# Kernel tuning notes

Hardware: AMD Instinct MI355X
Metric: run time of the kernel (lower is better)

The kernel has to match this reference:

```python
import jax, jax.numpy as jnp
import numpy as np

B, N, D = 8, 1024, 768
H, HD = 12, 64


def setup_inputs() -> dict:
    key = jax.random.key(0)
    ks = jax.random.split(key, 9)
    return {
        "x": jax.random.normal(ks[0], (B, N, D), dtype=jnp.float32),
        "Wq": jax.random.normal(ks[1], (H, HD, HD), dtype=jnp.float32) * (HD ** -0.5),
        "Wk": jax.random.normal(ks[2], (H, HD, HD), dtype=jnp.float32) * (HD ** -0.5),
        "Wv": jax.random.normal(ks[3], (H, HD, HD), dtype=jnp.float32) * (HD ** -0.5),
        "bq": jax.random.normal(ks[4], (H, HD), dtype=jnp.float32) * 0.02,
        "bk": jax.random.normal(ks[5], (H, HD), dtype=jnp.float32) * 0.02,
        "bv": jax.random.normal(ks[6], (H, HD), dtype=jnp.float32) * 0.02,
        "Wo": jax.random.normal(ks[7], (D, D), dtype=jnp.float32) * (D ** -0.5),
        "bo": jnp.zeros((D,), dtype=jnp.float32),
    }


def reference(x, Wq, Wk, Wv, bq, bk, bv, Wo, bo):
    # x: [B, N, D]; split into H heads of size HD along the feature dim
    b, n, d = x.shape
    h, hd = Wq.shape[0], Wq.shape[1]
    xh = x.reshape(b, n, h, hd)
    # per-head linear projections (stacked nn.Linear(head_dim, head_dim))
    q = jnp.einsum('bnhd,hde->bhne', xh, Wq) + bq[None, :, None, :]
    k = jnp.einsum('bnhd,hde->bhne', xh, Wk) + bk[None, :, None, :]
    v = jnp.einsum('bnhd,hde->bhne', xh, Wv) + bv[None, :, None, :]
    # NOTE: faithful quirk - scale uses FULL dim, not head_dim
    scale = d ** -0.5
    scores = jnp.einsum('bhid,bhjd->bhij', q, k) * scale  # [B,H,N,N]
    attn = jax.nn.softmax(scores, axis=-1)
    out = jnp.einsum('bhij,bhjd->bhid', attn, v)  # [B,H,N,HD]
    out = out.transpose(0, 2, 1, 3).reshape(b, n, d)  # concat heads
    return out @ Wo.T + bo  # wO: nn.Linear(dim, dim)
```

## Files before the change

### kernel.cpp

```cpp
#include <hip/hip_runtime.h>


typedef __attribute__((ext_vector_type(8))) short short8;
typedef __attribute__((ext_vector_type(4))) float floatx4;

#define MFMA16(a, b, c) __builtin_amdgcn_mfma_f32_16x16x32_bf16((a), (b), (c), 0, 0, 0)

#if __has_builtin(__builtin_amdgcn_exp2f)
#define EXP2(x) __builtin_amdgcn_exp2f(x)
#else
#define EXP2(x) __expf(0.6931471805599453f * (x))
#endif
#if __has_builtin(__builtin_amdgcn_rcpf)
#define RCP(x) __builtin_amdgcn_rcpf(x)
#else
#define RCP(x) (1.0f / (x))
#endif

__device__ __forceinline__ unsigned short f2bf(float f) {
    union { float f; unsigned int i; } c;
    c.f = f;
    unsigned int i = c.i;
    return (unsigned short)((i + 0x7fffu + ((i >> 16) & 1u)) >> 16);
}
__device__ __forceinline__ unsigned short f2bf_trunc(float f) {
    union { float f; unsigned int i; } c;
    c.f = f;
    return (unsigned short)(c.i >> 16);
}

__global__ __launch_bounds__(256) void prep_weights(
    const float* __restrict__ Wq, const float* __restrict__ Wk,
    const float* __restrict__ Wv, const float* __restrict__ Wo,
    unsigned short* __restrict__ Wqt, unsigned short* __restrict__ Wkt,
    unsigned short* __restrict__ Wvt, unsigned short* __restrict__ Wob)
{
    int tid = blockIdx.x * 256 + threadIdx.x;
    if (tid < 49152) {
        int h = tid >> 12, r = tid & 4095;
        int e = r >> 6, k = r & 63;
        int src = h * 4096 + k * 64 + e, dst = h * 4096 + e * 64 + k;
        Wqt[dst] = f2bf(Wq[src]);
        Wkt[dst] = f2bf(Wk[src]);
        Wvt[dst] = f2bf(Wv[src]);
    }
    for (int i = tid; i < 589824; i += 147456) Wob[i] = f2bf(Wo[i]);
}

__global__ __launch_bounds__(256) void qkv_proj(
    const float* __restrict__ x,
    const unsigned short* __restrict__ Wqt, const unsigned short* __restrict__ Wkt,
    const unsigned short* __restrict__ Wvt,
    const float* __restrict__ bq, const float* __restrict__ bk,
    const float* __restrict__ bv,
    unsigned short* __restrict__ Q, unsigned short* __restrict__ K,
    unsigned short* __restrict__ Vt)
{
    __shared__ __align__(16) unsigned short xlds[64 * 72];
    __shared__ __align__(16) unsigned short vlds[64 * 72];

    const int bh = blockIdx.y;
    const int b = bh / 12, h = bh % 12;
    const int wave = threadIdx.x >> 6, lane = threadIdx.x & 63;
    const int lrow = lane & 15, quad = lane >> 4;
    const int row0 = blockIdx.x * 64;
    const float scale = 0.052058776672f;

    {
        const int tr = threadIdx.x >> 4;
        const int tc = (threadIdx.x & 15) * 4;
        #pragma unroll
        for (int rr = 0; rr < 4; ++rr) {
            const int r = tr + rr * 16;
            const float* src = x + ((size_t)(b * 1024 + row0 + r)) * 768
                               + h * 64 + tc;
            float4 f = *(const float4*)src;
            unsigned short pkd[4];
            pkd[0] = f2bf(f.x); pkd[1] = f2bf(f.y);
            pkd[2] = f2bf(f.z); pkd[3] = f2bf(f.w);
            *(uint2*)&xlds[r * 72 + tc] = *(uint2*)pkd;
        }
    }
    __syncthreads();

    short8 xb0 = *(const short8*)&xlds[(wave * 16 + lrow) * 72 + quad * 8];
    short8 xb1 = *(const short8*)&xlds[(wave * 16 + lrow) * 72 + 32 + quad * 8];

    const floatx4 zero = { 0.f, 0.f, 0.f, 0.f };

    const unsigned short* Wm[2] = { Wqt + h * 4096, Wkt + h * 4096 };
    const float* bm[2] = { bq + h * 64, bk + h * 64 };
    unsigned short* Om[2] = {
        Q + ((size_t)bh * 1024 + row0 + wave * 16 + lrow) * 64,
        K + ((size_t)bh * 1024 + row0 + wave * 16 + lrow) * 64 };
    #pragma unroll
    for (int m = 0; m < 2; ++m) {
        const unsigned short* W = Wm[m];
        #pragma unroll
        for (int t = 0; t < 4; ++t) {
            short8 wa0 = *(const short8*)(W + (t * 16 + lrow) * 64 + quad * 8);
            short8 wa1 = *(const short8*)(W + (t * 16 + lrow) * 64 + 32 + quad * 8);
            floatx4 acc = zero;
            acc = MFMA16(wa0, xb0, acc);
            acc = MFMA16(wa1, xb1, acc);
            float4 bias = *(const float4*)(bm[m] + t * 16 + quad * 4);
            const float bs[4] = { bias.x, bias.y, bias.z, bias.w };
            unsigned short pkd[4];
            #pragma unroll
            for (int r = 0; r < 4; ++r) {
                float v = acc[r] + bs[r];
                if (m == 0) v *= scale;
                pkd[r] = f2bf(v);
            }
            *(uint2*)(Om[m] + t * 16 + quad * 4) = *(uint2*)pkd;
        }
    }

    {
        const unsigned short* W = Wvt + h * 4096;
        const float* bvh = bv + h * 64;
        #pragma unroll
        for (int t = 0; t < 4; ++t) {
            short8 wa0 = *(const short8*)(W + (t * 16 + lrow) * 64 + quad * 8);
            short8 wa1 = *(const short8*)(W + (t * 16 + lrow) * 64 + 32 + quad * 8);
            floatx4 acc = zero;
            acc = MFMA16(wa0, xb0, acc);
            acc = MFMA16(wa1, xb1, acc);
            float4 bias = *(const float4*)(bvh + t * 16 + quad * 4);
            const float bs[4] = { bias.x, bias.y, bias.z, bias.w };
            #pragma unroll
            for (int r = 0; r < 4; ++r)
                vlds[(t * 16 + quad * 4 + r) * 72 + wave * 16 + lrow]
                    = f2bf(acc[r] + bs[r]);
        }
    }
    __syncthreads();
    {
        const int er = threadIdx.x >> 2;
        const int sc = threadIdx.x & 3;
        short8 v0 = *(const short8*)&vlds[er * 72 + sc * 16];
        short8 v1 = *(const short8*)&vlds[er * 72 + sc * 16 + 8];
        unsigned short* dst = Vt + (size_t)bh * 65536 + (size_t)er * 1024
                              + row0 + sc * 16;
        *(short8*)dst = v0;
        *(short8*)(dst + 8) = v1;
    }
}

__global__ __launch_bounds__(256) void attn_kernel(
    const unsigned short* __restrict__ Q, const unsigned short* __restrict__ K,
    const unsigned short* __restrict__ Vt, unsigned short* __restrict__ AO)
{
    __shared__ __align__(16) unsigned short Klds[64 * 72];
    __shared__ __align__(16) unsigned short Vlds[64 * 72];

    const int bh = (int)blockIdx.x + ((int)blockIdx.y >> 3) * 8;
    const int qb = blockIdx.y & 7;
    const int b = bh / 12, h = bh % 12;
    const int wave = threadIdx.x >> 6, lane = threadIdx.x & 63;
    const int lrow = lane & 15, quad = lane >> 4;
    const int qrow0 = qb * 128 + wave * 32;

    const unsigned short* Qb = Q + (size_t)bh * 65536;
    const unsigned short* Kb = K + (size_t)bh * 65536;
    const unsigned short* Vb = Vt + (size_t)bh * 65536;

    const int tch = threadIdx.x & 7, trow = threadIdx.x >> 3;
    const int slot0 = ((trow & 4) << 2) | ((trow >> 3) << 2) | (trow & 3);

    short8 aq[2][2];
    #pragma unroll
    for (int mm = 0; mm < 2; ++mm) {
        const unsigned short* qr = Qb + (size_t)(qrow0 + mm * 16 + lrow) * 64;
        aq[mm][0] = *(const short8*)(qr + quad * 8);
        aq[mm][1] = *(const short8*)(qr + 32 + quad * 8);
    }

    const floatx4 zero = { 0.f, 0.f, 0.f, 0.f };
    float part[2] = { 0.f, 0.f };
    floatx4 Oacc[2][4];
    #pragma unroll
    for (int mm = 0; mm < 2; ++mm)
        #pragma unroll
        for (int t = 0; t < 4; ++t) Oacc[mm][t] = zero;

    short8 kpre[2], vpre[2];
    kpre[0] = *(const short8*)(Kb + (size_t)trow * 64 + tch * 8);
    kpre[1] = *(const short8*)(Kb + (size_t)(trow + 32) * 64 + tch * 8);
    vpre[0] = *(const short8*)(Vb + (size_t)trow * 1024 + tch * 8);
    vpre[1] = *(const short8*)(Vb + (size_t)(trow + 32) * 1024 + tch * 8);

    for (int jt = 0; jt < 16; ++jt) {
        *(short8*)&Klds[slot0 * 72 + tch * 8] = kpre[0];
        *(short8*)&Klds[(slot0 + 32) * 72 + tch * 8] = kpre[1];
        *(short8*)&Vlds[trow * 72 + tch * 8] = vpre[0];
        *(short8*)&Vlds[(trow + 32) * 72 + tch * 8] = vpre[1];
        __syncthreads();

        {
            const int jn = ((jt + 1) & 15) * 64;
            kpre[0] = *(const short8*)(Kb + (size_t)(jn + trow) * 64 + tch * 8);
            kpre[1] = *(const short8*)(Kb + (size_t)(jn + trow + 32) * 64 + tch * 8);
            vpre[0] = *(const short8*)(Vb + (size_t)trow * 1024 + jn + tch * 8);
            vpre[1] = *(const short8*)(Vb + (size_t)(trow + 32) * 1024 + jn + tch * 8);
        }

        #pragma unroll
        for (int w = 0; w < 2; ++w) {
            short8 kA[2][2];
            #pragma unroll
            for (int tau = 0; tau < 2; ++tau) {
                int kr = w * 32 + tau * 16 + lrow;
                kA[tau][0] = *(const short8*)&Klds[kr * 72 + quad * 8];
                kA[tau][1] = *(const short8*)&Klds[kr * 72 + 32 + quad * 8];
            }
            short8 vA[4];
            #pragma unroll
            for (int t = 0; t < 4; ++t)
                vA[t] = *(const short8*)&Vlds[(t * 16 + lrow) * 72
                                              + w * 32 + quad * 8];

            #pragma unroll
            for (int mm = 0; mm < 2; ++mm) {
                floatx4 s0 = zero, s1 = zero;
                s0 = MFMA16(kA[0][0], aq[mm][0], s0);
                s0 = MFMA16(kA[0][1], aq[mm][1], s0);
                s1 = MFMA16(kA[1][0], aq[mm][0], s1);
                s1 = MFMA16(kA[1][1], aq[mm][1], s1);

                short8 pk;
                #pragma unroll
                for (int r = 0; r < 4; ++r) {
                    float p0 = EXP2(s0[r]);
                    float p1 = EXP2(s1[r]);
                    part[mm] += p0 + p1;
                    pk[r] = (short)f2bf_trunc(p0);
                    pk[4 + r] = (short)f2bf_trunc(p1);
                }
                #pragma unroll
                for (int t = 0; t < 4; ++t)
                    Oacc[mm][t] = MFMA16(vA[t], pk, Oacc[mm][t]);
            }
        }
        __syncthreads();
    }

    #pragma unroll
    for (int mm = 0; mm < 2; ++mm) {
        float ts = part[mm];
        ts += __shfl_xor(ts, 16);
        ts += __shfl_xor(ts, 32);
        float inv = RCP(ts);
        unsigned short* orow = AO
            + ((size_t)(b * 1024 + qrow0 + mm * 16 + lrow)) * 768 + h * 64;
        #pragma unroll
        for (int t = 0; t < 4; ++t) {
            unsigned short pkd[4];
            #pragma unroll
            for (int r = 0; r < 4; ++r)
                pkd[r] = f2bf(Oacc[mm][t][r] * inv);
            *(uint2*)(orow + t * 16 + quad * 4) = *(uint2*)pkd;
        }
    }
}

__global__ __launch_bounds__(256) void out_proj(
    const unsigned short* __restrict__ AO, const unsigned short* __restrict__ Wob,
    const float* __restrict__ bo, float* __restrict__ Y)
{
    __shared__ __align__(16) unsigned short Alds[128 * 72];
    __shared__ __align__(16) unsigned short Blds[64 * 72];

    const int wave = threadIdx.x >> 6, lane = threadIdx.x & 63;
    const int lrow = lane & 15, quad = lane >> 4;
    const int row0 = blockIdx.x * 128;
    const int c0 = blockIdx.y * 64;
    const int wrow = (wave >> 1) * 64, wcol = (wave & 1) * 32;

    const int tch = threadIdx.x & 7, trow = threadIdx.x >> 3;

    const floatx4 zero = { 0.f, 0.f, 0.f, 0.f };
    floatx4 acc[2][4];
    #pragma unroll
    for (int u = 0; u < 2; ++u)
        #pragma unroll
        for (int t = 0; t < 4; ++t) acc[u][t] = zero;

    short8 apre[4], bpre[2];
    #pragma unroll
    for (int rr = 0; rr < 4; ++rr)
        apre[rr] = *(const short8*)(AO + (size_t)(row0 + trow + rr * 32) * 768
                                    + tch * 8);
    #pragma unroll
    for (int rr = 0; rr < 2; ++rr)
        bpre[rr] = *(const short8*)(Wob + (size_t)(c0 + trow + rr * 32) * 768
                                    + tch * 8);

    for (int k0 = 0; k0 < 768; k0 += 64) {
        #pragma unroll
        for (int rr = 0; rr < 4; ++rr)
            *(short8*)&Alds[(trow + rr * 32) * 72 + tch * 8] = apre[rr];
        #pragma unroll
        for (int rr = 0; rr < 2; ++rr)
            *(short8*)&Blds[(trow + rr * 32) * 72 + tch * 8] = bpre[rr];
        __syncthreads();

        {
            const int kn = (k0 + 64 < 768) ? k0 + 64 : 0;
            #pragma unroll
            for (int rr = 0; rr < 4; ++rr)
                apre[rr] = *(const short8*)(AO
                    + (size_t)(row0 + trow + rr * 32) * 768 + kn + tch * 8);
            #pragma unroll
            for (int rr = 0; rr < 2; ++rr)
                bpre[rr] = *(const short8*)(Wob
                    + (size_t)(c0 + trow + rr * 32) * 768 + kn + tch * 8);
        }

        #pragma unroll
        for (int kc = 0; kc < 2; ++kc) {
            short8 aoF[4], wF[2];
            #pragma unroll
            for (int t = 0; t < 4; ++t)
                aoF[t] = *(const short8*)&Alds[(wrow + t * 16 + lrow) * 72
                                               + kc * 32 + quad * 8];
            #pragma unroll
            for (int u = 0; u < 2; ++u)
                wF[u] = *(const short8*)&Blds[(wcol + u * 16 + lrow) * 72
                                              + kc * 32 + quad * 8];
            #pragma unroll
            for (int u = 0; u < 2; ++u)
                #pragma unroll
                for (int t = 0; t < 4; ++t)
                    acc[u][t] = MFMA16(wF[u], aoF[t], acc[u][t]);
        }
        __syncthreads();
    }

    #pragma unroll
    for (int u = 0; u < 2; ++u) {
        const int cb = c0 + wcol + u * 16 + quad * 4;
        float4 bias = *(const float4*)(bo + cb);
        const float bs[4] = { bias.x, bias.y, bias.z, bias.w };
        #pragma unroll
        for (int t = 0; t < 4; ++t) {
            const int row = row0 + wrow + t * 16 + lrow;
            float out[4];
            #pragma unroll
            for (int r = 0; r < 4; ++r) out[r] = acc[u][t][r] + bs[r];
            *(float4*)(Y + (size_t)row * 768 + cb) = *(float4*)out;
        }
    }
}

extern "C" void kernel_launch(void* const* d_in, const int* in_sizes, int n_in,
                              void* d_out, int out_size, void* d_ws, size_t ws_size,
                              hipStream_t stream)
{
    const float* x  = (const float*)d_in[0];
    const float* Wq = (const float*)d_in[1];
    const float* Wk = (const float*)d_in[2];
    const float* Wv = (const float*)d_in[3];
    const float* bq = (const float*)d_in[4];
    const float* bk = (const float*)d_in[5];
    const float* bv = (const float*)d_in[6];
    const float* Wo = (const float*)d_in[7];
    const float* bo = (const float*)d_in[8];

    unsigned short* Q   = (unsigned short*)d_ws;
    unsigned short* K   = Q + 6291456;
    unsigned short* Vt  = K + 6291456;
    unsigned short* AO  = Vt + 6291456;
    unsigned short* Wqt = AO + 6291456;
    unsigned short* Wkt = Wqt + 49152;
    unsigned short* Wvt = Wkt + 49152;
    unsigned short* Wob = Wvt + 49152;
    float* Y = (float*)d_out;

    prep_weights<<<dim3(576), 256, 0, stream>>>(Wq, Wk, Wv, Wo, Wqt, Wkt, Wvt, Wob);
    qkv_proj<<<dim3(16, 96), 256, 0, stream>>>(x, Wqt, Wkt, Wvt, bq, bk, bv, Q, K, Vt);
    attn_kernel<<<dim3(8, 96), 256, 0, stream>>>(Q, K, Vt, AO);
    out_proj<<<dim3(64, 12), 256, 0, stream>>>(AO, Wob, bo, Y);
}
```

Before: 169.9 us.

## Compute softmax row sums via MFMA with ones, packed bf16 cvt, wider out_proj tiles

In the attention kernel, the probability row sums are now accumulated with an extra MFMA against a bf16 ones vector instead of per-lane scalar adds plus cross-lane shuffles. The sum is taken over the bf16-rounded probabilities, which makes it consistent with what feeds the PV product. Probability conversion now uses the hardware packed v_cvt_pk_bf16_f32 instruction (round-to-nearest) instead of manual truncation. Separately, the output projection tile widens from 64 to 96 columns per block, cutting the grid from 12 to 8 column blocks, which gives more reuse per A load at the cost of more registers and LDS.

```diff
diff --git a/kernel.cpp b/kernel.cpp
--- a/kernel.cpp
+++ b/kernel.cpp
@@ -23,11 +23,6 @@
     unsigned int i = c.i;
     return (unsigned short)((i + 0x7fffu + ((i >> 16) & 1u)) >> 16);
 }
-__device__ __forceinline__ unsigned short f2bf_trunc(float f) {
-    union { float f; unsigned int i; } c;
-    c.f = f;
-    return (unsigned short)(c.i >> 16);
-}
 
 __global__ __launch_bounds__(256) void prep_weights(
     const float* __restrict__ Wq, const float* __restrict__ Wk,
@@ -177,7 +172,10 @@
     }
 
     const floatx4 zero = { 0.f, 0.f, 0.f, 0.f };
-    float part[2] = { 0.f, 0.f };
+    const short one_bf = (short)0x3F80;
+    const short8 ones8 = { one_bf, one_bf, one_bf, one_bf,
+                           one_bf, one_bf, one_bf, one_bf };
+    floatx4 Sacc[2] = { zero, zero };
     floatx4 Oacc[2][4];
     #pragma unroll
     for (int mm = 0; mm < 2; ++mm)
@@ -228,15 +226,20 @@
                 s1 = MFMA16(kA[1][0], aq[mm][0], s1);
                 s1 = MFMA16(kA[1][1], aq[mm][1], s1);
 
+                float p00 = EXP2(s0[0]), p01 = EXP2(s0[1]);
+                float p02 = EXP2(s0[2]), p03 = EXP2(s0[3]);
+                float p10 = EXP2(s1[0]), p11 = EXP2(s1[1]);
+                float p12 = EXP2(s1[2]), p13 = EXP2(s1[3]);
+                unsigned int w0, w1, w2, w3;
+                asm("v_cvt_pk_bf16_f32 %0, %1, %2" : "=v"(w0) : "v"(p00), "v"(p01));
+                asm("v_cvt_pk_bf16_f32 %0, %1, %2" : "=v"(w1) : "v"(p02), "v"(p03));
+                asm("v_cvt_pk_bf16_f32 %0, %1, %2" : "=v"(w2) : "v"(p10), "v"(p11));
+                asm("v_cvt_pk_bf16_f32 %0, %1, %2" : "=v"(w3) : "v"(p12), "v"(p13));
                 short8 pk;
-                #pragma unroll
-                for (int r = 0; r < 4; ++r) {
-                    float p0 = EXP2(s0[r]);
-                    float p1 = EXP2(s1[r]);
-                    part[mm] += p0 + p1;
-                    pk[r] = (short)f2bf_trunc(p0);
-                    pk[4 + r] = (short)f2bf_trunc(p1);
-                }
+                unsigned int* pw = (unsigned int*)&pk;
+                pw[0] = w0; pw[1] = w1; pw[2] = w2; pw[3] = w3;
+
+                Sacc[mm] = MFMA16(ones8, pk, Sacc[mm]);
                 #pragma unroll
                 for (int t = 0; t < 4; ++t)
                     Oacc[mm][t] = MFMA16(vA[t], pk, Oacc[mm][t]);
@@ -247,10 +250,7 @@
 
     #pragma unroll
     for (int mm = 0; mm < 2; ++mm) {
-        float ts = part[mm];
-        ts += __shfl_xor(ts, 16);
-        ts += __shfl_xor(ts, 32);
-        float inv = RCP(ts);
+        float inv = RCP(Sacc[mm][0]);
         unsigned short* orow = AO
             + ((size_t)(b * 1024 + qrow0 + mm * 16 + lrow)) * 768 + h * 64;
         #pragma unroll
@@ -269,30 +269,30 @@
     const float* __restrict__ bo, float* __restrict__ Y)
 {
     __shared__ __align__(16) unsigned short Alds[128 * 72];
-    __shared__ __align__(16) unsigned short Blds[64 * 72];
+    __shared__ __align__(16) unsigned short Blds[96 * 72];
 
     const int wave = threadIdx.x >> 6, lane = threadIdx.x & 63;
     const int lrow = lane & 15, quad = lane >> 4;
     const int row0 = blockIdx.x * 128;
-    const int c0 = blockIdx.y * 64;
-    const int wrow = (wave >> 1) * 64, wcol = (wave & 1) * 32;
+    const int c0 = blockIdx.y * 96;
+    const int wrow = (wave >> 1) * 64, wcol = (wave & 1) * 48;
 
     const int tch = threadIdx.x & 7, trow = threadIdx.x >> 3;
 
     const floatx4 zero = { 0.f, 0.f, 0.f, 0.f };
-    floatx4 acc[2][4];
-    #pragma unroll
-    for (int u = 0; u < 2; ++u)
+    floatx4 acc[3][4];
+    #pragma unroll
+    for (int u = 0; u < 3; ++u)
         #pragma unroll
         for (int t = 0; t < 4; ++t) acc[u][t] = zero;
 
-    short8 apre[4], bpre[2];
+    short8 apre[4], bpre[3];
     #pragma unroll
     for (int rr = 0; rr < 4; ++rr)
         apre[rr] = *(const short8*)(AO + (size_t)(row0 + trow + rr * 32) * 768
                                     + tch * 8);
     #pragma unroll
-    for (int rr = 0; rr < 2; ++rr)
+    for (int rr = 0; rr < 3; ++rr)
         bpre[rr] = *(const short8*)(Wob + (size_t)(c0 + trow + rr * 32) * 768
                                     + tch * 8);
 
@@ -301,7 +301,7 @@
         for (int rr = 0; rr < 4; ++rr)
             *(short8*)&Alds[(trow + rr * 32) * 72 + tch * 8] = apre[rr];
         #pragma unroll
-        for (int rr = 0; rr < 2; ++rr)
+        for (int rr = 0; rr < 3; ++rr)
             *(short8*)&Blds[(trow + rr * 32) * 72 + tch * 8] = bpre[rr];
         __syncthreads();
 
@@ -312,24 +312,24 @@
                 apre[rr] = *(const short8*)(AO
                     + (size_t)(row0 + trow + rr * 32) * 768 + kn + tch * 8);
             #pragma unroll
-            for (int rr = 0; rr < 2; ++rr)
+            for (int rr = 0; rr < 3; ++rr)
                 bpre[rr] = *(const short8*)(Wob
                     + (size_t)(c0 + trow + rr * 32) * 768 + kn + tch * 8);
         }
 
         #pragma unroll
         for (int kc = 0; kc < 2; ++kc) {
-            short8 aoF[4], wF[2];
+            short8 aoF[4], wF[3];
             #pragma unroll
             for (int t = 0; t < 4; ++t)
                 aoF[t] = *(const short8*)&Alds[(wrow + t * 16 + lrow) * 72
                                                + kc * 32 + quad * 8];
             #pragma unroll
-            for (int u = 0; u < 2; ++u)
+            for (int u = 0; u < 3; ++u)
                 wF[u] = *(const short8*)&Blds[(wcol + u * 16 + lrow) * 72
                                               + kc * 32 + quad * 8];
             #pragma unroll
-            for (int u = 0; u < 2; ++u)
+            for (int u = 0; u < 3; ++u)
                 #pragma unroll
                 for (int t = 0; t < 4; ++t)
                     acc[u][t] = MFMA16(wF[u], aoF[t], acc[u][t]);
@@ -338,7 +338,7 @@
     }
 
     #pragma unroll
-    for (int u = 0; u < 2; ++u) {
+    for (int u = 0; u < 3; ++u) {
         const int cb = c0 + wcol + u * 16 + quad * 4;
         float4 bias = *(const float4*)(bo + cb);
         const float bs[4] = { bias.x, bias.y, bias.z, bias.w };
@@ -380,5 +380,5 @@
     prep_weights<<<dim3(576), 256, 0, stream>>>(Wq, Wk, Wv, Wo, Wqt, Wkt, Wvt, Wob);
     qkv_proj<<<dim3(16, 96), 256, 0, stream>>>(x, Wqt, Wkt, Wvt, bq, bk, bv, Q, K, Vt);
     attn_kernel<<<dim3(8, 96), 256, 0, stream>>>(Q, K, Vt, AO);
-    out_proj<<<dim3(64, 12), 256, 0, stream>>>(AO, Wob, bo, Y);
-}
+    out_proj<<<dim3(64, 8), 256, 0, stream>>>(AO, Wob, bo, Y);
+}
```

Result: no change. 170.3 us (+0.3%).

## Double-buffer K in LDS, load V fragments from global, widen out_proj tiles

Applied to the files above, without the earlier changes.

The attention kernel now double-buffers the K tile in LDS, which leaves one barrier per iteration instead of two. It stops staging V through LDS and has each wave read its MFMA operand fragments straight from global memory (L2/L1). Separately, out_proj tiles grow from 64 to 96 output columns per block, giving fewer blocks and more reuse of the A tile. The risks are uncoalesced global V reads on the critical path and higher register pressure in both kernels.

```diff
diff --git a/kernel.cpp b/kernel.cpp
--- a/kernel.cpp
+++ b/kernel.cpp
@@ -151,8 +151,7 @@
     const unsigned short* __restrict__ Q, const unsigned short* __restrict__ K,
     const unsigned short* __restrict__ Vt, unsigned short* __restrict__ AO)
 {
-    __shared__ __align__(16) unsigned short Klds[64 * 72];
-    __shared__ __align__(16) unsigned short Vlds[64 * 72];
+    __shared__ __align__(16) unsigned short Klds[2][64 * 72];
 
     const int bh = (int)blockIdx.x + ((int)blockIdx.y >> 3) * 8;
     const int qb = blockIdx.y & 7;
@@ -184,41 +183,48 @@
         #pragma unroll
         for (int t = 0; t < 4; ++t) Oacc[mm][t] = zero;
 
-    short8 kpre[2], vpre[2];
+    short8 kpre[2];
     kpre[0] = *(const short8*)(Kb + (size_t)trow * 64 + tch * 8);
     kpre[1] = *(const short8*)(Kb + (size_t)(trow + 32) * 64 + tch * 8);
-    vpre[0] = *(const short8*)(Vb + (size_t)trow * 1024 + tch * 8);
-    vpre[1] = *(const short8*)(Vb + (size_t)(trow + 32) * 1024 + tch * 8);
+    *(short8*)&Klds[0][slot0 * 72 + tch * 8] = kpre[0];
+    *(short8*)&Klds[0][(slot0 + 32) * 72 + tch * 8] = kpre[1];
+    kpre[0] = *(const short8*)(Kb + (size_t)(64 + trow) * 64 + tch * 8);
+    kpre[1] = *(const short8*)(Kb + (size_t)(64 + trow + 32) * 64 + tch * 8);
 
     for (int jt = 0; jt < 16; ++jt) {
-        *(short8*)&Klds[slot0 * 72 + tch * 8] = kpre[0];
-        *(short8*)&Klds[(slot0 + 32) * 72 + tch * 8] = kpre[1];
-        *(short8*)&Vlds[trow * 72 + tch * 8] = vpre[0];
-        *(short8*)&Vlds[(trow + 32) * 72 + tch * 8] = vpre[1];
         __syncthreads();
 
         {
-            const int jn = ((jt + 1) & 15) * 64;
+            unsigned short* kb = (unsigned short*)Klds[(jt + 1) & 1];
+            *(short8*)&kb[slot0 * 72 + tch * 8] = kpre[0];
+            *(short8*)&kb[(slot0 + 32) * 72 + tch * 8] = kpre[1];
+        }
+        {
+            const int jn = ((jt + 2) & 15) * 64;
             kpre[0] = *(const short8*)(Kb + (size_t)(jn + trow) * 64 + tch * 8);
             kpre[1] = *(const short8*)(Kb + (size_t)(jn + trow + 32) * 64 + tch * 8);
-            vpre[0] = *(const short8*)(Vb + (size_t)trow * 1024 + jn + tch * 8);
-            vpre[1] = *(const short8*)(Vb + (size_t)(trow + 32) * 1024 + jn + tch * 8);
-        }
-
+        }
+        short8 vA[2][4];
+        {
+            const int jv = jt * 64;
+            #pragma unroll
+            for (int w = 0; w < 2; ++w)
+                #pragma unroll
+                for (int t = 0; t < 4; ++t)
+                    vA[w][t] = *(const short8*)(Vb
+                        + (size_t)(t * 16 + lrow) * 1024 + jv + w * 32 + quad * 8);
+        }
+
+        const unsigned short* kbuf = (const unsigned short*)Klds[jt & 1];
         #pragma unroll
         for (int w = 0; w < 2; ++w) {
             short8 kA[2][2];
             #pragma unroll
             for (int tau = 0; tau < 2; ++tau) {
                 int kr = w * 32 + tau * 16 + lrow;
-                kA[tau][0] = *(const short8*)&Klds[kr * 72 + quad * 8];
-                kA[tau][1] = *(const short8*)&Klds[kr * 72 + 32 + quad * 8];
+                kA[tau][0] = *(const short8*)&kbuf[kr * 72 + quad * 8];
+                kA[tau][1] = *(const short8*)&kbuf[kr * 72 + 32 + quad * 8];
             }
-            short8 vA[4];
-            #pragma unroll
-            for (int t = 0; t < 4; ++t)
-                vA[t] = *(const short8*)&Vlds[(t * 16 + lrow) * 72
-                                              + w * 32 + quad * 8];
 
             #pragma unroll
             for (int mm = 0; mm < 2; ++mm) {
@@ -239,10 +245,9 @@
                 }
                 #pragma unroll
                 for (int t = 0; t < 4; ++t)
-                    Oacc[mm][t] = MFMA16(vA[t], pk, Oacc[mm][t]);
+                    Oacc[mm][t] = MFMA16(vA[w][t], pk, Oacc[mm][t]);
             }
         }
-        __syncthreads();
     }
 
     #pragma unroll
@@ -269,30 +274,30 @@
     const float* __restrict__ bo, float* __restrict__ Y)
 {
     __shared__ __align__(16) unsigned short Alds[128 * 72];
-    __shared__ __align__(16) unsigned short Blds[64 * 72];
+    __shared__ __align__(16) unsigned short Blds[96 * 72];
 
     const int wave = threadIdx.x >> 6, lane = threadIdx.x & 63;
     const int lrow = lane & 15, quad = lane >> 4;
     const int row0 = blockIdx.x * 128;
-    const int c0 = blockIdx.y * 64;
-    const int wrow = (wave >> 1) * 64, wcol = (wave & 1) * 32;
+    const int c0 = blockIdx.y * 96;
+    const int wrow = (wave >> 1) * 64, wcol = (wave & 1) * 48;
 
     const int tch = threadIdx.x & 7, trow = threadIdx.x >> 3;
 
     const floatx4 zero = { 0.f, 0.f, 0.f, 0.f };
-    floatx4 acc[2][4];
-    #pragma unroll
-    for (int u = 0; u < 2; ++u)
+    floatx4 acc[3][4];
+    #pragma unroll
+    for (int u = 0; u < 3; ++u)
         #pragma unroll
         for (int t = 0; t < 4; ++t) acc[u][t] = zero;
 
-    short8 apre[4], bpre[2];
+    short8 apre[4], bpre[3];
     #pragma unroll
     for (int rr = 0; rr < 4; ++rr)
         apre[rr] = *(const short8*)(AO + (size_t)(row0 + trow + rr * 32) * 768
                                     + tch * 8);
     #pragma unroll
-    for (int rr = 0; rr < 2; ++rr)
+    for (int rr = 0; rr < 3; ++rr)
         bpre[rr] = *(const short8*)(Wob + (size_t)(c0 + trow + rr * 32) * 768
                                     + tch * 8);
 
@@ -301,7 +306,7 @@
         for (int rr = 0; rr < 4; ++rr)
             *(short8*)&Alds[(trow + rr * 32) * 72 + tch * 8] = apre[rr];
         #pragma unroll
-        for (int rr = 0; rr < 2; ++rr)
+        for (int rr = 0; rr < 3; ++rr)
             *(short8*)&Blds[(trow + rr * 32) * 72 + tch * 8] = bpre[rr];
         __syncthreads();
 
@@ -312,24 +317,24 @@
                 apre[rr] = *(const short8*)(AO
                     + (size_t)(row0 + trow + rr * 32) * 768 + kn + tch * 8);
             #pragma unroll
-            for (int rr = 0; rr < 2; ++rr)
+            for (int rr = 0; rr < 3; ++rr)
                 bpre[rr] = *(const short8*)(Wob
                     + (size_t)(c0 + trow + rr * 32) * 768 + kn + tch * 8);
         }
 
         #pragma unroll
         for (int kc = 0; kc < 2; ++kc) {
-            short8 aoF[4], wF[2];
+            short8 aoF[4], wF[3];
             #pragma unroll
             for (int t = 0; t < 4; ++t)
                 aoF[t] = *(const short8*)&Alds[(wrow + t * 16 + lrow) * 72
                                                + kc * 32 + quad * 8];
             #pragma unroll
-            for (int u = 0; u < 2; ++u)
+            for (int u = 0; u < 3; ++u)
                 wF[u] = *(const short8*)&Blds[(wcol + u * 16 + lrow) * 72
                                               + kc * 32 + quad * 8];
             #pragma unroll
-            for (int u = 0; u < 2; ++u)
+            for (int u = 0; u < 3; ++u)
                 #pragma unroll
                 for (int t = 0; t < 4; ++t)
                     acc[u][t] = MFMA16(wF[u], aoF[t], acc[u][t]);
@@ -338,7 +343,7 @@
     }
 
     #pragma unroll
-    for (int u = 0; u < 2; ++u) {
+    for (int u = 0; u < 3; ++u) {
         const int cb = c0 + wcol + u * 16 + quad * 4;
         float4 bias = *(const float4*)(bo + cb);
         const float bs[4] = { bias.x, bias.y, bias.z, bias.w };
@@ -380,5 +385,5 @@
     prep_weights<<<dim3(576), 256, 0, stream>>>(Wq, Wk, Wv, Wo, Wqt, Wkt, Wvt, Wob);
     qkv_proj<<<dim3(16, 96), 256, 0, stream>>>(x, Wqt, Wkt, Wvt, bq, bk, bv, Q, K, Vt);
     attn_kernel<<<dim3(8, 96), 256, 0, stream>>>(Q, K, Vt, AO);
-    out_proj<<<dim3(64, 12), 256, 0, stream>>>(AO, Wob, bo, Y);
-}
+    out_proj<<<dim3(64, 8), 256, 0, stream>>>(AO, Wob, bo, Y);
+}
```

After: 184.7 us. 1.09x slower.
